# Performance work log

Measured on AMD Instinct MI355X. Metric: run time of the kernel, lower is better.

The kernel has to match this reference:

```python
import jax, jax.numpy as jnp
import numpy as np


def setup_inputs() -> dict:
    key = jax.random.key(0)
    k1, k2, k3 = jax.random.split(key, 3)
    B, H, N, D = 4, 4, 4096, 64
    q = jax.random.normal(k1, (B, H, N, D), dtype=jnp.float32)
    k = jax.random.normal(k2, (B, H, N, D), dtype=jnp.float32)
    v = jax.random.normal(k3, (B, H, N, D), dtype=jnp.float32)
    return {"q": q, "k": k, "v": v}


def reference(q, k, v):
    # eager QK^T softmax V attention, scale = d^{-1/2}
    scale = q.shape[-1] ** (-0.5)
    sim = jnp.einsum('...id,...jd->...ij', q, k) * scale  # [B,H,N,N]
    attention = jax.nn.softmax(sim, axis=-1)
    output = jnp.einsum('...ij,...jd->...id', attention, v)  # [B,H,N,D]
    return (output, attention)
```

## Files before the change

kernel.cpp:

```cpp
#include <hip/hip_runtime.h>

#define N_CTX 4096
#define DHEAD 64
#define NBH   16
#define LDK   40
#define LDKK  72

typedef _Float16 half8 __attribute__((ext_vector_type(8)));
typedef float    f32x4 __attribute__((ext_vector_type(4)));

__global__ __launch_bounds__(256, 4)
void attn_fused(const float* __restrict__ Q, const float* __restrict__ K,
                const float* __restrict__ V, float* __restrict__ out)
{
    const int bh     = blockIdx.y;
    const int rowblk = blockIdx.x;
    const int tid  = threadIdx.x;
    const int wave = tid >> 6;
    const int lane = tid & 63;
    const int l15  = lane & 15;
    const int quad = lane >> 4;

    __shared__ __attribute__((aligned(16))) _Float16 s_k[32 * LDKK];
    __shared__ __attribute__((aligned(16))) _Float16 s_v[64 * LDK];
    __shared__ __attribute__((aligned(16))) _Float16 s_p[4][16 * LDK];

    const size_t base = (size_t)bh * N_CTX * DHEAD;
    const int gr0 = rowblk * 64 + wave * 16;

    half8 aq[2];
    {
        const float* qp = Q + base + (size_t)(gr0 + l15) * DHEAD;
        #pragma unroll
        for (int h = 0; h < 2; ++h) {
            const float4 f0 = *(const float4*)(qp + 32*h + 8*quad);
            const float4 f1 = *(const float4*)(qp + 32*h + 8*quad + 4);
            half8 a;
            a[0]=(_Float16)(f0.x*0.125f); a[1]=(_Float16)(f0.y*0.125f);
            a[2]=(_Float16)(f0.z*0.125f); a[3]=(_Float16)(f0.w*0.125f);
            a[4]=(_Float16)(f1.x*0.125f); a[5]=(_Float16)(f1.y*0.125f);
            a[6]=(_Float16)(f1.z*0.125f); a[7]=(_Float16)(f1.w*0.125f);
            aq[h] = a;
        }
    }

    const int st_key = tid >> 3, st_c  = tid & 7;
    const int sv_d   = tid >> 2, sv_kc = tid & 3;

    f32x4 oacc[4] = {{0.f,0.f,0.f,0.f},{0.f,0.f,0.f,0.f},
                     {0.f,0.f,0.f,0.f},{0.f,0.f,0.f,0.f}};
    float lacc[4] = {0.f, 0.f, 0.f, 0.f};

    for (int jt = 0; jt < N_CTX / 32; ++jt) {
        const int j0 = jt * 32;
        __syncthreads();
        {
            const float* kp = K + base + (size_t)(j0 + st_key) * DHEAD + 8*st_c;
            const float4 f0 = *(const float4*)kp;
            const float4 f1 = *(const float4*)(kp + 4);
            half8 a;
            a[0]=(_Float16)f0.x; a[1]=(_Float16)f0.y; a[2]=(_Float16)f0.z; a[3]=(_Float16)f0.w;
            a[4]=(_Float16)f1.x; a[5]=(_Float16)f1.y; a[6]=(_Float16)f1.z; a[7]=(_Float16)f1.w;
            *(half8*)&s_k[st_key * LDKK + 8*st_c] = a;
        }
        {
            const float* vp = V + base + (size_t)(j0 + 8*sv_kc) * DHEAD + sv_d;
            half8 a;
            #pragma unroll
            for (int j = 0; j < 8; ++j) a[j] = (_Float16)vp[j * DHEAD];
            *(half8*)&s_v[sv_d * LDK + 8*sv_kc] = a;
        }
        __syncthreads();

        f32x4 sc[2];
        #pragma unroll
        for (int jj = 0; jj < 2; ++jj) {
            const half8 b0 = *(const half8*)&s_k[(16*jj + l15) * LDKK + 8*quad];
            const half8 b1 = *(const half8*)&s_k[(16*jj + l15) * LDKK + 32 + 8*quad];
            f32x4 acc = {0.f,0.f,0.f,0.f};
            acc = __builtin_amdgcn_mfma_f32_16x16x32_f16(aq[0], b0, acc, 0, 0, 0);
            acc = __builtin_amdgcn_mfma_f32_16x16x32_f16(aq[1], b1, acc, 0, 0, 0);
            sc[jj] = acc;
        }
        #pragma unroll
        for (int jj = 0; jj < 2; ++jj)
            #pragma unroll
            for (int r = 0; r < 4; ++r) {
                const float p = __expf(sc[jj][r]);
                lacc[r] += p;
                s_p[wave][(4*quad + r) * LDK + 16*jj + l15] = (_Float16)p;
            }
        __syncthreads();
        const half8 ap = *(const half8*)&s_p[wave][l15 * LDK + 8*quad];
        #pragma unroll
        for (int dt = 0; dt < 4; ++dt) {
            const half8 bv = *(const half8*)&s_v[(16*dt + l15) * LDK + 8*quad];
            oacc[dt] = __builtin_amdgcn_mfma_f32_16x16x32_f16(ap, bv, oacc[dt], 0, 0, 0);
        }
    }

    float inv[4];
    #pragma unroll
    for (int r = 0; r < 4; ++r) {
        float s = lacc[r];
        s += __shfl_xor(s, 1); s += __shfl_xor(s, 2);
        s += __shfl_xor(s, 4); s += __shfl_xor(s, 8);
        inv[r] = 1.0f / s;
    }

    {
        float* op = out + base + (size_t)gr0 * DHEAD;
        #pragma unroll
        for (int dt = 0; dt < 4; ++dt)
            #pragma unroll
            for (int r = 0; r < 4; ++r)
                op[(size_t)(4*quad + r) * DHEAD + 16*dt + l15] = oacc[dt][r] * inv[r];
    }

    float* ap_out = out + (size_t)NBH * N_CTX * DHEAD
                  + (size_t)bh * N_CTX * N_CTX + (size_t)gr0 * N_CTX;
    for (int jt = 0; jt < N_CTX / 32; ++jt) {
        const int j0 = jt * 32;
        __syncthreads();
        {
            const float* kp = K + base + (size_t)(j0 + st_key) * DHEAD + 8*st_c;
            const float4 f0 = *(const float4*)kp;
            const float4 f1 = *(const float4*)(kp + 4);
            half8 a;
            a[0]=(_Float16)f0.x; a[1]=(_Float16)f0.y; a[2]=(_Float16)f0.z; a[3]=(_Float16)f0.w;
            a[4]=(_Float16)f1.x; a[5]=(_Float16)f1.y; a[6]=(_Float16)f1.z; a[7]=(_Float16)f1.w;
            *(half8*)&s_k[st_key * LDKK + 8*st_c] = a;
        }
        __syncthreads();
        #pragma unroll
        for (int jj = 0; jj < 2; ++jj) {
            const half8 b0 = *(const half8*)&s_k[(16*jj + l15) * LDKK + 8*quad];
            const half8 b1 = *(const half8*)&s_k[(16*jj + l15) * LDKK + 32 + 8*quad];
            f32x4 acc = {0.f,0.f,0.f,0.f};
            acc = __builtin_amdgcn_mfma_f32_16x16x32_f16(aq[0], b0, acc, 0, 0, 0);
            acc = __builtin_amdgcn_mfma_f32_16x16x32_f16(aq[1], b1, acc, 0, 0, 0);
            #pragma unroll
            for (int r = 0; r < 4; ++r)
                ap_out[(size_t)(4*quad + r) * N_CTX + j0 + 16*jj + l15]
                    = __expf(acc[r]) * inv[r];
        }
    }
}

extern "C" void kernel_launch(void* const* d_in, const int* in_sizes, int n_in,
                              void* d_out, int out_size, void* d_ws, size_t ws_size,
                              hipStream_t stream)
{
    const float* q = (const float*)d_in[0];
    const float* k = (const float*)d_in[1];
    const float* v = (const float*)d_in[2];
    float* o = (float*)d_out;
    dim3 grid(N_CTX / 64, NBH), block(256);
    hipLaunchKernelGGL(attn_fused, grid, block, 0, stream, q, k, v, o);
}
```

Measured before the change: 1.459 ms.

## Enlarge key tile, prefetch K/V into registers, transpose MFMA for vector stores

Key tiles grow from 32 to 64, and the next tile's K/V loads are issued into registers before the current tile's compute so global latency overlaps the MFMAs. Operands of the MFMA are swapped so each lane owns a row and consecutive columns, allowing float4 nontemporal stores of the attention matrix and output. The block-wide barrier before the P·V step is replaced by a per-wave LDS waitcnt, and blocks are remapped across heads. This adds register pressure from the prefetch buffers and relies on a hand-placed waitcnt for correctness.

```diff
diff --git a/kernel.cpp b/kernel.cpp
--- a/kernel.cpp
+++ b/kernel.cpp
@@ -3,27 +3,31 @@
 #define N_CTX 4096
 #define DHEAD 64
 #define NBH   16
-#define LDK   40
-#define LDKK  72
+#define NT    (N_CTX / 64)
+#define LDT   72
 
 typedef _Float16 half8 __attribute__((ext_vector_type(8)));
+typedef _Float16 half4 __attribute__((ext_vector_type(4)));
 typedef float    f32x4 __attribute__((ext_vector_type(4)));
 
 __global__ __launch_bounds__(256, 4)
 void attn_fused(const float* __restrict__ Q, const float* __restrict__ K,
                 const float* __restrict__ V, float* __restrict__ out)
 {
-    const int bh     = blockIdx.y;
-    const int rowblk = blockIdx.x;
     const int tid  = threadIdx.x;
     const int wave = tid >> 6;
     const int lane = tid & 63;
     const int l15  = lane & 15;
     const int quad = lane >> 4;
 
-    __shared__ __attribute__((aligned(16))) _Float16 s_k[32 * LDKK];
-    __shared__ __attribute__((aligned(16))) _Float16 s_v[64 * LDK];
-    __shared__ __attribute__((aligned(16))) _Float16 s_p[4][16 * LDK];
+    const int dd     = blockIdx.y * 64 + blockIdx.x;
+    const int c      = dd >> 3;
+    const int bh     = 2 * (dd & 7) + (c >> 6);
+    const int rowblk = c & 63;
+
+    __shared__ __attribute__((aligned(16))) _Float16 s_k[64 * LDT];
+    __shared__ __attribute__((aligned(16))) _Float16 s_v[64 * LDT];
+    __shared__ __attribute__((aligned(16))) _Float16 s_p[4][16 * LDT];
 
     const size_t base = (size_t)bh * N_CTX * DHEAD;
     const int gr0 = rowblk * 64 + wave * 16;
@@ -44,105 +48,122 @@
         }
     }
 
-    const int st_key = tid >> 3, st_c  = tid & 7;
-    const int sv_d   = tid >> 2, sv_kc = tid & 3;
+    const int st_row = tid >> 2;
+    const int st_c   = (tid & 3) * 16;
+    const float* kp = K + base + (size_t)st_row * DHEAD + st_c;
+    const float* vp = V + base + (size_t)st_c  * DHEAD + st_row;
+
+    float4 kf[4];
+    float  vf[16];
+    #pragma unroll
+    for (int q = 0; q < 4; ++q) kf[q] = *(const float4*)(kp + 4*q);
+    #pragma unroll
+    for (int j = 0; j < 16; ++j) vf[j] = vp[(size_t)j * DHEAD];
 
     f32x4 oacc[4] = {{0.f,0.f,0.f,0.f},{0.f,0.f,0.f,0.f},
                      {0.f,0.f,0.f,0.f},{0.f,0.f,0.f,0.f}};
-    float lacc[4] = {0.f, 0.f, 0.f, 0.f};
+    float lacc = 0.f;
+    _Float16* const sp = &s_p[wave][0];
 
-    for (int jt = 0; jt < N_CTX / 32; ++jt) {
-        const int j0 = jt * 32;
-        __syncthreads();
-        {
-            const float* kp = K + base + (size_t)(j0 + st_key) * DHEAD + 8*st_c;
-            const float4 f0 = *(const float4*)kp;
-            const float4 f1 = *(const float4*)(kp + 4);
-            half8 a;
-            a[0]=(_Float16)f0.x; a[1]=(_Float16)f0.y; a[2]=(_Float16)f0.z; a[3]=(_Float16)f0.w;
-            a[4]=(_Float16)f1.x; a[5]=(_Float16)f1.y; a[6]=(_Float16)f1.z; a[7]=(_Float16)f1.w;
-            *(half8*)&s_k[st_key * LDKK + 8*st_c] = a;
-        }
-        {
-            const float* vp = V + base + (size_t)(j0 + 8*sv_kc) * DHEAD + sv_d;
-            half8 a;
-            #pragma unroll
-            for (int j = 0; j < 8; ++j) a[j] = (_Float16)vp[j * DHEAD];
-            *(half8*)&s_v[sv_d * LDK + 8*sv_kc] = a;
-        }
-        __syncthreads();
-
-        f32x4 sc[2];
+    for (int jt = 0; jt < NT; ++jt) {
+        half8 kh0, kh1, vh0, vh1;
         #pragma unroll
-        for (int jj = 0; jj < 2; ++jj) {
-            const half8 b0 = *(const half8*)&s_k[(16*jj + l15) * LDKK + 8*quad];
-            const half8 b1 = *(const half8*)&s_k[(16*jj + l15) * LDKK + 32 + 8*quad];
-            f32x4 acc = {0.f,0.f,0.f,0.f};
-            acc = __builtin_amdgcn_mfma_f32_16x16x32_f16(aq[0], b0, acc, 0, 0, 0);
-            acc = __builtin_amdgcn_mfma_f32_16x16x32_f16(aq[1], b1, acc, 0, 0, 0);
-            sc[jj] = acc;
+        for (int i = 0; i < 4; ++i) {
+            kh0[i]   = (_Float16)kf[0][i]; kh0[i+4] = (_Float16)kf[1][i];
+            kh1[i]   = (_Float16)kf[2][i]; kh1[i+4] = (_Float16)kf[3][i];
         }
         #pragma unroll
-        for (int jj = 0; jj < 2; ++jj)
+        for (int i = 0; i < 8; ++i) { vh0[i] = (_Float16)vf[i]; vh1[i] = (_Float16)vf[i+8]; }
+        __syncthreads();
+        *(half8*)&s_k[st_row * LDT + st_c    ] = kh0;
+        *(half8*)&s_k[st_row * LDT + st_c + 8] = kh1;
+        *(half8*)&s_v[st_row * LDT + st_c    ] = vh0;
+        *(half8*)&s_v[st_row * LDT + st_c + 8] = vh1;
+        __syncthreads();
+        if (jt + 1 < NT) {
+            kp += 64 * DHEAD; vp += 64 * DHEAD;
+            #pragma unroll
+            for (int q = 0; q < 4; ++q) kf[q] = *(const float4*)(kp + 4*q);
+            #pragma unroll
+            for (int j = 0; j < 16; ++j) vf[j] = vp[(size_t)j * DHEAD];
+        }
+        #pragma unroll
+        for (int jj = 0; jj < 4; ++jj) {
+            const half8 b0 = *(const half8*)&s_k[(16*jj + l15) * LDT + 8*quad];
+            const half8 b1 = *(const half8*)&s_k[(16*jj + l15) * LDT + 32 + 8*quad];
+            f32x4 acc = {0.f,0.f,0.f,0.f};
+            acc = __builtin_amdgcn_mfma_f32_16x16x32_f16(b0, aq[0], acc, 0, 0, 0);
+            acc = __builtin_amdgcn_mfma_f32_16x16x32_f16(b1, aq[1], acc, 0, 0, 0);
+            half4 ph;
             #pragma unroll
             for (int r = 0; r < 4; ++r) {
-                const float p = __expf(sc[jj][r]);
-                lacc[r] += p;
-                s_p[wave][(4*quad + r) * LDK + 16*jj + l15] = (_Float16)p;
+                const float p = __expf(acc[r]);
+                lacc += p;
+                ph[r] = (_Float16)p;
             }
-        __syncthreads();
-        const half8 ap = *(const half8*)&s_p[wave][l15 * LDK + 8*quad];
+            *(half4*)&sp[l15 * LDT + 16*jj + 4*quad] = ph;
+        }
+        __asm__ volatile("s_waitcnt lgkmcnt(0)" ::: "memory");
+        __builtin_amdgcn_sched_barrier(0);
+        const half8 ap0 = *(const half8*)&sp[l15 * LDT + 8*quad];
+        const half8 ap1 = *(const half8*)&sp[l15 * LDT + 32 + 8*quad];
         #pragma unroll
         for (int dt = 0; dt < 4; ++dt) {
-            const half8 bv = *(const half8*)&s_v[(16*dt + l15) * LDK + 8*quad];
-            oacc[dt] = __builtin_amdgcn_mfma_f32_16x16x32_f16(ap, bv, oacc[dt], 0, 0, 0);
+            const half8 bv0 = *(const half8*)&s_v[(16*dt + l15) * LDT + 8*quad];
+            const half8 bv1 = *(const half8*)&s_v[(16*dt + l15) * LDT + 32 + 8*quad];
+            oacc[dt] = __builtin_amdgcn_mfma_f32_16x16x32_f16(bv0, ap0, oacc[dt], 0, 0, 0);
+            oacc[dt] = __builtin_amdgcn_mfma_f32_16x16x32_f16(bv1, ap1, oacc[dt], 0, 0, 0);
         }
     }
 
-    float inv[4];
-    #pragma unroll
-    for (int r = 0; r < 4; ++r) {
-        float s = lacc[r];
-        s += __shfl_xor(s, 1); s += __shfl_xor(s, 2);
-        s += __shfl_xor(s, 4); s += __shfl_xor(s, 8);
-        inv[r] = 1.0f / s;
+    lacc += __shfl_xor(lacc, 16);
+    lacc += __shfl_xor(lacc, 32);
+    const float inv = 1.0f / lacc;
+
+    {
+        float* op = out + base + (size_t)(gr0 + l15) * DHEAD;
+        #pragma unroll
+        for (int dt = 0; dt < 4; ++dt) {
+            f32x4 ov;
+            #pragma unroll
+            for (int r = 0; r < 4; ++r) ov[r] = oacc[dt][r] * inv;
+            __builtin_nontemporal_store(ov, (f32x4*)(op + 16*dt + 4*quad));
+        }
     }
 
-    {
-        float* op = out + base + (size_t)gr0 * DHEAD;
+    kp = K + base + (size_t)st_row * DHEAD + st_c;
+    #pragma unroll
+    for (int q = 0; q < 4; ++q) kf[q] = *(const float4*)(kp + 4*q);
+    float* const arow = out + (size_t)NBH * N_CTX * DHEAD
+                      + (size_t)bh * N_CTX * N_CTX + (size_t)(gr0 + l15) * N_CTX;
+    for (int jt = 0; jt < NT; ++jt) {
+        half8 kh0, kh1;
         #pragma unroll
-        for (int dt = 0; dt < 4; ++dt)
-            #pragma unroll
-            for (int r = 0; r < 4; ++r)
-                op[(size_t)(4*quad + r) * DHEAD + 16*dt + l15] = oacc[dt][r] * inv[r];
-    }
-
-    float* ap_out = out + (size_t)NBH * N_CTX * DHEAD
-                  + (size_t)bh * N_CTX * N_CTX + (size_t)gr0 * N_CTX;
-    for (int jt = 0; jt < N_CTX / 32; ++jt) {
-        const int j0 = jt * 32;
-        __syncthreads();
-        {
-            const float* kp = K + base + (size_t)(j0 + st_key) * DHEAD + 8*st_c;
-            const float4 f0 = *(const float4*)kp;
-            const float4 f1 = *(const float4*)(kp + 4);
-            half8 a;
-            a[0]=(_Float16)f0.x; a[1]=(_Float16)f0.y; a[2]=(_Float16)f0.z; a[3]=(_Float16)f0.w;
-            a[4]=(_Float16)f1.x; a[5]=(_Float16)f1.y; a[6]=(_Float16)f1.z; a[7]=(_Float16)f1.w;
-            *(half8*)&s_k[st_key * LDKK + 8*st_c] = a;
+        for (int i = 0; i < 4; ++i) {
+            kh0[i]   = (_Float16)kf[0][i]; kh0[i+4] = (_Float16)kf[1][i];
+            kh1[i]   = (_Float16)kf[2][i]; kh1[i+4] = (_Float16)kf[3][i];
         }
         __syncthreads();
+        *(half8*)&s_k[st_row * LDT + st_c    ] = kh0;
+        *(half8*)&s_k[st_row * LDT + st_c + 8] = kh1;
+        __syncthreads();
+        if (jt + 1 < NT) {
+            kp += 64 * DHEAD;
+            #pragma unroll
+            for (int q = 0; q < 4; ++q) kf[q] = *(const float4*)(kp + 4*q);
+        }
+        const int j0 = jt * 64;
         #pragma unroll
-        for (int jj = 0; jj < 2; ++jj) {
-            const half8 b0 = *(const half8*)&s_k[(16*jj + l15) * LDKK + 8*quad];
-            const half8 b1 = *(const half8*)&s_k[(16*jj + l15) * LDKK + 32 + 8*quad];
+        for (int jj = 0; jj < 4; ++jj) {
+            const half8 b0 = *(const half8*)&s_k[(16*jj + l15) * LDT + 8*quad];
+            const half8 b1 = *(const half8*)&s_k[(16*jj + l15) * LDT + 32 + 8*quad];
             f32x4 acc = {0.f,0.f,0.f,0.f};
-            acc = __builtin_amdgcn_mfma_f32_16x16x32_f16(aq[0], b0, acc, 0, 0, 0);
-            acc = __builtin_amdgcn_mfma_f32_16x16x32_f16(aq[1], b1, acc, 0, 0, 0);
+            acc = __builtin_amdgcn_mfma_f32_16x16x32_f16(b0, aq[0], acc, 0, 0, 0);
+            acc = __builtin_amdgcn_mfma_f32_16x16x32_f16(b1, aq[1], acc, 0, 0, 0);
+            f32x4 av;
             #pragma unroll
-            for (int r = 0; r < 4; ++r)
-                ap_out[(size_t)(4*quad + r) * N_CTX + j0 + 16*jj + l15]
-                    = __expf(acc[r]) * inv[r];
+            for (int r = 0; r < 4; ++r) av[r] = __expf(acc[r]) * inv;
+            __builtin_nontemporal_store(av, (f32x4*)(arow + j0 + 16*jj + 4*quad));
         }
     }
 }
```

New measurement: 1.352 ms. -7.4%, faster.
